# Kernel tuning notes

Hardware: AMD Instinct MI355X
Metric: run time of the kernel (lower is better)

The kernel has to match this reference:

```python
import jax, jax.numpy as jnp
import numpy as np

B, H, W, C = 32, 64, 64, 384
WS = 8            # window size (square)
NH = 12           # num heads
HD = C // NH      # head dim
SCALE = HD ** -0.5


def setup_inputs() -> dict:
    key = jax.random.key(0)
    ks = jax.random.split(key, 5)
    std = 0.02
    return {
        "x": jax.random.normal(ks[0], (B, H, W, C), dtype=jnp.float32),
        "w_qkv": jax.random.normal(ks[1], (C, 3 * C), dtype=jnp.float32) * std,
        "b_qkv": jnp.zeros((3 * C,), dtype=jnp.float32),
        "w_proj": jax.random.normal(ks[2], (C, C), dtype=jnp.float32) * std,
        "b_proj": jnp.zeros((C,), dtype=jnp.float32),
    }


def reference(x, w_qkv, b_qkv, w_proj, b_proj):
    b, h, w, c = x.shape
    nh_win, nw_win = h // WS, w // WS
    # window partition: (B, nh, WS, nw, WS, C) -> (B*nw_total, WS*WS, C)
    xw = x.reshape(b, nh_win, WS, nw_win, WS, c)
    xw = xw.transpose(0, 1, 3, 2, 4, 5).reshape(b * nh_win * nw_win, WS * WS, c)
    nW, T = xw.shape[0], WS * WS
    # qkv projection
    qkv = xw @ w_qkv + b_qkv                      # (nW, T, 3C)
    qkv = qkv.reshape(nW, T, 3, NH, HD).transpose(2, 0, 3, 1, 4)
    q, k, v = qkv[0], qkv[1], qkv[2]              # (nW, NH, T, HD)
    attn = jnp.einsum('wntd,wnsd->wnts', q, k) * SCALE
    attn = jax.nn.softmax(attn, axis=-1)
    out = jnp.einsum('wnts,wnsd->wntd', attn, v)  # (nW, NH, T, HD)
    out = out.transpose(0, 2, 1, 3).reshape(nW, T, c)
    out = out @ w_proj + b_proj
    # window reverse
    out = out.reshape(b, nh_win, nw_win, WS, WS, c)
    out = out.transpose(0, 1, 3, 2, 4, 5).reshape(b, h, w, c)
    return out
```

## Files before the change

kernel.cpp:

```cpp
#include <hip/hip_runtime.h>
#include <hip/hip_bf16.h>

typedef __bf16 bfv8 __attribute__((ext_vector_type(8)));
typedef float f32x4 __attribute__((ext_vector_type(4)));
typedef unsigned int u32;

#define MFMA(a,b,c) __builtin_amdgcn_mfma_f32_16x16x32_bf16((a),(b),(c),0,0,0)

constexpr int XW_LD = 392;

__global__ __launch_bounds__(256)
void prep_weights(const float* __restrict__ w_qkv, const float* __restrict__ w_proj,
                  unsigned short* __restrict__ qT, unsigned short* __restrict__ pT)
{
    int i = blockIdx.x * 256 + threadIdx.x;
    const int NQ = 1152 * 384;
    if (i < NQ) {
        int c = i / 384, k = i - c * 384;
        __bf16 h = (__bf16)w_qkv[k * 1152 + c];
        qT[i] = *(unsigned short*)&h;
    } else {
        int j = i - NQ;
        if (j < 384 * 384) {
            int c = j / 384, k = j - c * 384;
            __bf16 h = (__bf16)w_proj[k * 384 + c];
            pT[j] = *(unsigned short*)&h;
        }
    }
}

__device__ __forceinline__ u32 pkbf(float a, float b) {
    __bf16 x = (__bf16)a, y = (__bf16)b;
    unsigned short lo = *(unsigned short*)&x, hi = *(unsigned short*)&y;
    return ((u32)hi << 16) | lo;
}

__device__ __forceinline__ bfv8 conv_frag(u32 p00, u32 p01, u32 p10, u32 p11,
                                          int abase, bool selhi)
{
    union { u32 u[4]; bfv8 v; } cv;
    #pragma unroll
    for (int w = 0; w < 4; ++w) {
        const int addr = abase + (w >> 1) * 64;
        const int lo_ = __builtin_amdgcn_ds_bpermute(addr, (int)((w & 1) ? p01 : p00));
        const int hi_ = __builtin_amdgcn_ds_bpermute(addr, (int)((w & 1) ? p11 : p10));
        cv.u[w] = (u32)(selhi ? hi_ : lo_);
    }
    return cv.v;
}

__global__ __launch_bounds__(256, 3)
void win_attn(const float* __restrict__ x,
              const float* __restrict__ b_qkv,
              const float* __restrict__ b_proj,
              const unsigned short* __restrict__ qT_,
              const unsigned short* __restrict__ pT_,
              float* __restrict__ out)
{
    __shared__ __bf16 sX[64 * XW_LD];

    const __bf16* wqkvT  = (const __bf16*)qT_;
    const __bf16* wprojT = (const __bf16*)pT_;

    const int wid  = blockIdx.x;
    const int bb   = wid >> 6;
    const int wy   = (wid >> 3) & 7;
    const int wx   = wid & 7;
    const int tid  = threadIdx.x;
    const int lane = tid & 63;
    const int wv   = tid >> 6;
    const int lr   = lane & 15;
    const int lg   = lane >> 4;
    const int k8   = lg * 8;

    const size_t gbase = ((size_t)(bb * 64 + wy * 8) * 64 + wx * 8) * 384;

    {
        const float* xb = x + gbase;
        for (int i = tid; i < 64 * 96; i += 256) {
            int t  = i / 96;
            int c4 = (i - t * 96) * 4;
            const float4 v = *(const float4*)(xb + (size_t)((t >> 3) * 64 + (t & 7)) * 384 + c4);
            *(uint2*)&sX[t * XW_LD + c4] = make_uint2(pkbf(v.x, v.y), pkbf(v.z, v.w));
        }
    }
    __syncthreads();

    const int   abase = ((lg & 1) * 32 + lr) * 4;
    const bool  selhi = (lg & 2) != 0;
    const float SC    = 0.17677669529663687f;

    u32 opk0[4][2][2], opk1[4][2][2], opk2[4][2][2];

    auto head_body = [&](const int h, u32 (&opk_)[4][2][2]) {
        const int cQ = h * 32, cK = cQ + 384, cV = cQ + 768;

        f32x4 aq[2][4], ak[2][4], av[4][2];
        #pragma unroll
        for (int a = 0; a < 2; ++a)
            #pragma unroll
            for (int b = 0; b < 4; ++b) { aq[a][b] = f32x4{0,0,0,0}; ak[a][b] = f32x4{0,0,0,0}; av[b][a] = f32x4{0,0,0,0}; }

        const __bf16* wqp = wqkvT + (size_t)(cQ + lr) * 384 + k8;
        const __bf16* wkp = wqkvT + (size_t)(cK + lr) * 384 + k8;
        const __bf16* wvp = wqkvT + (size_t)(cV + lr) * 384 + k8;
        const __bf16* xp  = &sX[lr * XW_LD + k8];

        #pragma unroll 3
        for (int kk = 0; kk < 12; ++kk) {
            bfv8 xf[4], wqf[2], wkf[2], wvf[2];
            #pragma unroll
            for (int t4 = 0; t4 < 4; ++t4) xf[t4] = *(const bfv8*)(xp + t4 * 16 * XW_LD + kk * 32);
            #pragma unroll
            for (int hdt = 0; hdt < 2; ++hdt) {
                wqf[hdt] = *(const bfv8*)(wqp + (size_t)hdt * 16 * 384 + kk * 32);
                wkf[hdt] = *(const bfv8*)(wkp + (size_t)hdt * 16 * 384 + kk * 32);
                wvf[hdt] = *(const bfv8*)(wvp + (size_t)hdt * 16 * 384 + kk * 32);
            }
            __builtin_amdgcn_s_setprio(1);
            #pragma unroll
            for (int hdt = 0; hdt < 2; ++hdt)
                #pragma unroll
                for (int t4 = 0; t4 < 4; ++t4) {
                    aq[hdt][t4] = MFMA(wqf[hdt], xf[t4], aq[hdt][t4]);
                    ak[hdt][t4] = MFMA(wkf[hdt], xf[t4], ak[hdt][t4]);
                    av[t4][hdt] = MFMA(xf[t4], wvf[hdt], av[t4][hdt]);
                }
            __builtin_amdgcn_s_setprio(0);
        }

        float bqv[2][4], bkv[2][4], bvv[2];
        #pragma unroll
        for (int hdt = 0; hdt < 2; ++hdt) {
            #pragma unroll
            for (int r = 0; r < 4; ++r) {
                bqv[hdt][r] = b_qkv[cQ + hdt * 16 + lg * 4 + r];
                bkv[hdt][r] = b_qkv[cK + hdt * 16 + lg * 4 + r];
            }
            bvv[hdt] = b_qkv[cV + hdt * 16 + lr];
        }

        u32 pkQ[2][4][2], pkK[2][4][2], pkV[4][2][2];
        #pragma unroll
        for (int hdt = 0; hdt < 2; ++hdt)
            #pragma unroll
            for (int t4 = 0; t4 < 4; ++t4)
                #pragma unroll
                for (int p = 0; p < 2; ++p) {
                    pkQ[hdt][t4][p] = pkbf((aq[hdt][t4][2 * p] + bqv[hdt][2 * p]) * SC,
                                           (aq[hdt][t4][2 * p + 1] + bqv[hdt][2 * p + 1]) * SC);
                    pkK[hdt][t4][p] = pkbf(ak[hdt][t4][2 * p] + bkv[hdt][2 * p],
                                           ak[hdt][t4][2 * p + 1] + bkv[hdt][2 * p + 1]);
                    pkV[t4][hdt][p] = pkbf(av[t4][hdt][2 * p] + bvv[hdt],
                                           av[t4][hdt][2 * p + 1] + bvv[hdt]);
                }

        bfv8 Qf[4];
        #pragma unroll
        for (int qt = 0; qt < 4; ++qt)
            Qf[qt] = conv_frag(pkQ[0][qt][0], pkQ[0][qt][1], pkQ[1][qt][0], pkQ[1][qt][1], abase, selhi);
        f32x4 st[4][4];
        __builtin_amdgcn_s_setprio(1);
        #pragma unroll
        for (int kt = 0; kt < 4; ++kt) {
            const bfv8 kf = conv_frag(pkK[0][kt][0], pkK[0][kt][1], pkK[1][kt][0], pkK[1][kt][1], abase, selhi);
            #pragma unroll
            for (int qt = 0; qt < 4; ++qt) {
                f32x4 z{};
                st[kt][qt] = MFMA(kf, Qf[qt], z);
            }
        }
        __builtin_amdgcn_s_setprio(0);

        float rinv[4];
        #pragma unroll
        for (int qt = 0; qt < 4; ++qt) {
            float mx = -1e30f;
            #pragma unroll
            for (int kt = 0; kt < 4; ++kt)
                #pragma unroll
                for (int r = 0; r < 4; ++r) mx = fmaxf(mx, st[kt][qt][r]);
            mx = fmaxf(mx, __shfl_xor(mx, 16, 64));
            mx = fmaxf(mx, __shfl_xor(mx, 32, 64));
            float sum = 0.f;
            #pragma unroll
            for (int kt = 0; kt < 4; ++kt)
                #pragma unroll
                for (int r = 0; r < 4; ++r) { st[kt][qt][r] = __expf(st[kt][qt][r] - mx); sum += st[kt][qt][r]; }
            sum += __shfl_xor(sum, 16, 64);
            sum += __shfl_xor(sum, 32, 64);
            rinv[qt] = 1.f / sum;
        }
        u32 pkP[4][4][2];
        #pragma unroll
        for (int qt = 0; qt < 4; ++qt)
            #pragma unroll
            for (int kt = 0; kt < 4; ++kt)
                #pragma unroll
                for (int p = 0; p < 2; ++p)
                    pkP[qt][kt][p] = pkbf(st[kt][qt][2 * p] * rinv[qt], st[kt][qt][2 * p + 1] * rinv[qt]);

        bfv8 Vf[2][2];
        #pragma unroll
        for (int ks = 0; ks < 2; ++ks)
            #pragma unroll
            for (int hdt = 0; hdt < 2; ++hdt)
                Vf[ks][hdt] = conv_frag(pkV[2 * ks][hdt][0], pkV[2 * ks][hdt][1],
                                        pkV[2 * ks + 1][hdt][0], pkV[2 * ks + 1][hdt][1], abase, selhi);
        f32x4 o[4][2];
        #pragma unroll
        for (int qt = 0; qt < 4; ++qt)
            #pragma unroll
            for (int hdt = 0; hdt < 2; ++hdt) o[qt][hdt] = f32x4{0,0,0,0};
        #pragma unroll
        for (int qt = 0; qt < 4; ++qt) {
            bfv8 pf0 = conv_frag(pkP[qt][0][0], pkP[qt][0][1], pkP[qt][1][0], pkP[qt][1][1], abase, selhi);
            bfv8 pf1 = conv_frag(pkP[qt][2][0], pkP[qt][2][1], pkP[qt][3][0], pkP[qt][3][1], abase, selhi);
            __builtin_amdgcn_s_setprio(1);
            #pragma unroll
            for (int hdt = 0; hdt < 2; ++hdt) {
                o[qt][hdt] = MFMA(pf0, Vf[0][hdt], o[qt][hdt]);
                o[qt][hdt] = MFMA(pf1, Vf[1][hdt], o[qt][hdt]);
            }
            __builtin_amdgcn_s_setprio(0);
        }
        #pragma unroll
        for (int qt = 0; qt < 4; ++qt)
            #pragma unroll
            for (int hdt = 0; hdt < 2; ++hdt)
                #pragma unroll
                for (int p = 0; p < 2; ++p)
                    opk_[qt][hdt][p] = pkbf(o[qt][hdt][2 * p], o[qt][hdt][2 * p + 1]);
    };

    head_body(wv * 3 + 0, opk0);
    head_body(wv * 3 + 1, opk1);
    head_body(wv * 3 + 2, opk2);

    __syncthreads();

#define OWRITE(OPK, HL)                                                          \
    _Pragma("unroll") for (int qt = 0; qt < 4; ++qt)                             \
    _Pragma("unroll") for (int hdt = 0; hdt < 2; ++hdt)                          \
    _Pragma("unroll") for (int p = 0; p < 2; ++p) {                              \
        const u32 u = OPK[qt][hdt][p];                                           \
        const int row0 = qt * 16 + lg * 4 + 2 * p;                               \
        const int col  = (wv * 3 + (HL)) * 32 + hdt * 16 + lr;                   \
        unsigned short lo = (unsigned short)(u & 0xffff);                        \
        unsigned short hi = (unsigned short)(u >> 16);                           \
        sX[row0 * XW_LD + col]       = *(__bf16*)&lo;                            \
        sX[(row0 + 1) * XW_LD + col] = *(__bf16*)&hi;                            \
    }
    OWRITE(opk0, 0)
    OWRITE(opk1, 1)
    OWRITE(opk2, 2)
    __syncthreads();

    const int nb = wv * 96;
    f32x4 acc[4][6];
    {
        const __bf16* bp = wprojT + (size_t)(nb + lr) * 384 + k8;
        #pragma unroll
        for (int m = 0; m < 4; ++m)
            #pragma unroll
            for (int nt = 0; nt < 6; ++nt) acc[m][nt] = f32x4{0,0,0,0};
        #pragma unroll 2
        for (int kk = 0; kk < 12; ++kk) {
            bfv8 bfr[6];
            #pragma unroll
            for (int nt = 0; nt < 6; ++nt)
                bfr[nt] = *(const bfv8*)(bp + (size_t)nt * 16 * 384 + kk * 32);
            __builtin_amdgcn_s_setprio(1);
            #pragma unroll
            for (int m = 0; m < 4; ++m) {
                const bfv8 af = *(const bfv8*)&sX[(m * 16 + lr) * XW_LD + kk * 32 + k8];
                #pragma unroll
                for (int nt = 0; nt < 6; ++nt)
                    acc[m][nt] = MFMA(af, bfr[nt], acc[m][nt]);
            }
            __builtin_amdgcn_s_setprio(0);
        }
    }
    float bpj[6];
    #pragma unroll
    for (int nt = 0; nt < 6; ++nt) bpj[nt] = b_proj[nb + nt * 16 + lr];

    __syncthreads();
    float* sF = (float*)sX;
    float* ob = out + gbase;
    #pragma unroll
    for (int half = 0; half < 2; ++half) {
        #pragma unroll
        for (int mm = 0; mm < 2; ++mm) {
            const int m = half * 2 + mm;
            #pragma unroll
            for (int r = 0; r < 4; ++r) {
                const int row = mm * 16 + lg * 4 + r;
                #pragma unroll
                for (int nt = 0; nt < 6; ++nt)
                    sF[row * 384 + nb + nt * 16 + lr] = acc[m][nt][r] + bpj[nt];
            }
        }
        __syncthreads();
        for (int i = tid; i < 32 * 96; i += 256) {
            const int row = i / 96;
            const int c4  = (i - row * 96) * 4;
            const int t   = half * 32 + row;
            const float4 v = *(const float4*)&sF[row * 384 + c4];
            *(float4*)(ob + (size_t)((t >> 3) * 64 + (t & 7)) * 384 + c4) = v;
        }
        if (half == 0) __syncthreads();
    }
}

extern "C" void kernel_launch(void* const* d_in, const int* in_sizes, int n_in,
                              void* d_out, int out_size, void* d_ws, size_t ws_size,
                              hipStream_t stream)
{
    const float* x      = (const float*)d_in[0];
    const float* w_qkv  = (const float*)d_in[1];
    const float* b_qkv  = (const float*)d_in[2];
    const float* w_proj = (const float*)d_in[3];
    const float* b_proj = (const float*)d_in[4];
    float* out = (float*)d_out;

    unsigned short* qT = (unsigned short*)d_ws;
    unsigned short* pT = qT + 1152 * 384;

    const int NPREP = 1152 * 384 + 384 * 384;
    prep_weights<<<(NPREP + 255) / 256, 256, 0, stream>>>(w_qkv, w_proj, qT, pT);
    win_attn<<<2048, 256, 0, stream>>>(x, b_qkv, b_proj, qT, pT, out);
}
```

Baseline: 386.9 us.

## Stage weight tiles through LDS with async global_load_lds and double-buffered register prefetch

Weight fragments for the QKV and output projections are now fetched with global_load_lds into a per-wave LDS staging buffer. They are then read into registers through a software-pipelined double buffer, with explicit waitcnt and sched_barrier ordering so the next k-slice's loads overlap the current MFMAs. The per-head lambda becomes a non-unrolled loop, and occupancy hint drops from 3 to 2 blocks per CU to accommodate the extra LDS and registers. The aim is to hide global-load latency behind MFMA work, at the cost of lower occupancy and heavy reliance on hand-placed wait counts.

```diff
diff --git a/kernel.cpp b/kernel.cpp
--- a/kernel.cpp
+++ b/kernel.cpp
@@ -6,6 +6,7 @@
 typedef unsigned int u32;
 
 #define MFMA(a,b,c) __builtin_amdgcn_mfma_f32_16x16x32_bf16((a),(b),(c),0,0,0)
+#define SB() __builtin_amdgcn_sched_barrier(0)
 
 constexpr int XW_LD = 392;
 
@@ -35,6 +36,12 @@
     return ((u32)hi << 16) | lo;
 }
 
+__device__ __forceinline__ void gll16(const __bf16* g, __bf16* l) {
+    __builtin_amdgcn_global_load_lds(
+        (const __attribute__((address_space(1))) void*)g,
+        (__attribute__((address_space(3))) void*)l, 16, 0, 0);
+}
+
 __device__ __forceinline__ bfv8 conv_frag(u32 p00, u32 p01, u32 p10, u32 p11,
                                           int abase, bool selhi)
 {
@@ -49,7 +56,7 @@
     return cv.v;
 }
 
-__global__ __launch_bounds__(256, 3)
+__global__ __launch_bounds__(256, 2)
 void win_attn(const float* __restrict__ x,
               const float* __restrict__ b_qkv,
               const float* __restrict__ b_proj,
@@ -58,6 +65,7 @@
               float* __restrict__ out)
 {
     __shared__ __bf16 sX[64 * XW_LD];
+    __shared__ __bf16 sW[4][6][512];
 
     const __bf16* wqkvT  = (const __bf16*)qT_;
     const __bf16* wprojT = (const __bf16*)pT_;
@@ -72,6 +80,7 @@
     const int lr   = lane & 15;
     const int lg   = lane >> 4;
     const int k8   = lg * 8;
+    const int lane8 = lane * 8;
 
     const size_t gbase = ((size_t)(bb * 64 + wy * 8) * 64 + wx * 8) * 384;
 
@@ -92,42 +101,19 @@
 
     u32 opk0[4][2][2], opk1[4][2][2], opk2[4][2][2];
 
-    auto head_body = [&](const int h, u32 (&opk_)[4][2][2]) {
+    const __bf16* xp = &sX[lr * XW_LD + k8];
+
+    #pragma unroll 1
+    for (int hl = 0; hl < 3; ++hl) {
+        const int h  = wv * 3 + hl;
         const int cQ = h * 32, cK = cQ + 384, cV = cQ + 768;
 
-        f32x4 aq[2][4], ak[2][4], av[4][2];
-        #pragma unroll
-        for (int a = 0; a < 2; ++a)
-            #pragma unroll
-            for (int b = 0; b < 4; ++b) { aq[a][b] = f32x4{0,0,0,0}; ak[a][b] = f32x4{0,0,0,0}; av[b][a] = f32x4{0,0,0,0}; }
-
-        const __bf16* wqp = wqkvT + (size_t)(cQ + lr) * 384 + k8;
-        const __bf16* wkp = wqkvT + (size_t)(cK + lr) * 384 + k8;
-        const __bf16* wvp = wqkvT + (size_t)(cV + lr) * 384 + k8;
-        const __bf16* xp  = &sX[lr * XW_LD + k8];
-
-        #pragma unroll 3
-        for (int kk = 0; kk < 12; ++kk) {
-            bfv8 xf[4], wqf[2], wkf[2], wvf[2];
-            #pragma unroll
-            for (int t4 = 0; t4 < 4; ++t4) xf[t4] = *(const bfv8*)(xp + t4 * 16 * XW_LD + kk * 32);
-            #pragma unroll
-            for (int hdt = 0; hdt < 2; ++hdt) {
-                wqf[hdt] = *(const bfv8*)(wqp + (size_t)hdt * 16 * 384 + kk * 32);
-                wkf[hdt] = *(const bfv8*)(wkp + (size_t)hdt * 16 * 384 + kk * 32);
-                wvf[hdt] = *(const bfv8*)(wvp + (size_t)hdt * 16 * 384 + kk * 32);
-            }
-            __builtin_amdgcn_s_setprio(1);
+        const __bf16* gsrc[6];
+        #pragma unroll
+        for (int mat = 0; mat < 3; ++mat)
             #pragma unroll
             for (int hdt = 0; hdt < 2; ++hdt)
-                #pragma unroll
-                for (int t4 = 0; t4 < 4; ++t4) {
-                    aq[hdt][t4] = MFMA(wqf[hdt], xf[t4], aq[hdt][t4]);
-                    ak[hdt][t4] = MFMA(wkf[hdt], xf[t4], ak[hdt][t4]);
-                    av[t4][hdt] = MFMA(xf[t4], wvf[hdt], av[t4][hdt]);
-                }
-            __builtin_amdgcn_s_setprio(0);
-        }
+                gsrc[mat * 2 + hdt] = wqkvT + (size_t)(cQ + mat * 384 + hdt * 16 + lr) * 384 + k8;
 
         float bqv[2][4], bkv[2][4], bvv[2];
         #pragma unroll
@@ -139,6 +125,57 @@
             }
             bvv[hdt] = b_qkv[cV + hdt * 16 + lr];
         }
+
+        f32x4 aq[2][4], ak[2][4], av[4][2];
+        #pragma unroll
+        for (int a = 0; a < 2; ++a)
+            #pragma unroll
+            for (int b = 0; b < 4; ++b) { aq[a][b] = f32x4{0,0,0,0}; ak[a][b] = f32x4{0,0,0,0}; av[b][a] = f32x4{0,0,0,0}; }
+
+        bfv8 wA[6], xA[4], wB[6], xB[4];
+
+        #pragma unroll
+        for (int f = 0; f < 6; ++f) gll16(gsrc[f], &sW[wv][f][0]);
+        asm volatile("s_waitcnt vmcnt(0)" ::: "memory"); SB();
+        #pragma unroll
+        for (int f = 0; f < 6; ++f) wA[f] = *(const bfv8*)&sW[wv][f][lane8];
+        #pragma unroll
+        for (int t4 = 0; t4 < 4; ++t4) xA[t4] = *(const bfv8*)(xp + t4 * 16 * XW_LD);
+        asm volatile("s_waitcnt lgkmcnt(4)" ::: "memory"); SB();
+        #pragma unroll
+        for (int f = 0; f < 6; ++f) gll16(gsrc[f] + 32, &sW[wv][f][0]);
+
+#define QSTEP(WA, XA, WB, XB, KK) do {                                            \
+        const int kread = ((KK) + 1 < 12) ? (KK) + 1 : 11;                        \
+        const int kpre  = ((KK) + 2 < 12) ? (KK) + 2 : 11;                        \
+        asm volatile("s_waitcnt vmcnt(0)" ::: "memory"); SB();                    \
+        _Pragma("unroll") for (int f = 0; f < 6; ++f)                             \
+            WB[f] = *(const bfv8*)&sW[wv][f][lane8];                              \
+        _Pragma("unroll") for (int t4 = 0; t4 < 4; ++t4)                          \
+            XB[t4] = *(const bfv8*)(xp + t4 * 16 * XW_LD + kread * 32);           \
+        __builtin_amdgcn_s_setprio(1);                                            \
+        _Pragma("unroll") for (int t4 = 0; t4 < 4; ++t4) {                        \
+            aq[0][t4] = MFMA(WA[0], XA[t4], aq[0][t4]);                           \
+            ak[0][t4] = MFMA(WA[2], XA[t4], ak[0][t4]);                           \
+            av[t4][0] = MFMA(XA[t4], WA[4], av[t4][0]); }                         \
+        __builtin_amdgcn_s_setprio(0);                                            \
+        asm volatile("s_waitcnt lgkmcnt(4)" ::: "memory"); SB();                  \
+        _Pragma("unroll") for (int f = 0; f < 6; ++f)                             \
+            gll16(gsrc[f] + kpre * 32, &sW[wv][f][0]);                            \
+        __builtin_amdgcn_s_setprio(1);                                            \
+        _Pragma("unroll") for (int t4 = 0; t4 < 4; ++t4) {                        \
+            aq[1][t4] = MFMA(WA[1], XA[t4], aq[1][t4]);                           \
+            ak[1][t4] = MFMA(WA[3], XA[t4], ak[1][t4]);                           \
+            av[t4][1] = MFMA(XA[t4], WA[5], av[t4][1]); }                         \
+        __builtin_amdgcn_s_setprio(0);                                            \
+    } while (0)
+
+        #pragma unroll 1
+        for (int kp = 0; kp < 6; ++kp) {
+            QSTEP(wA, xA, wB, xB, 2 * kp);
+            QSTEP(wB, xB, wA, xA, 2 * kp + 1);
+        }
+#undef QSTEP
 
         u32 pkQ[2][4][2], pkK[2][4][2], pkV[4][2][2];
         #pragma unroll
@@ -224,18 +261,25 @@
             }
             __builtin_amdgcn_s_setprio(0);
         }
+        u32 tmp[4][2][2];
         #pragma unroll
         for (int qt = 0; qt < 4; ++qt)
             #pragma unroll
             for (int hdt = 0; hdt < 2; ++hdt)
                 #pragma unroll
                 for (int p = 0; p < 2; ++p)
-                    opk_[qt][hdt][p] = pkbf(o[qt][hdt][2 * p], o[qt][hdt][2 * p + 1]);
-    };
-
-    head_body(wv * 3 + 0, opk0);
-    head_body(wv * 3 + 1, opk1);
-    head_body(wv * 3 + 2, opk2);
+                    tmp[qt][hdt][p] = pkbf(o[qt][hdt][2 * p], o[qt][hdt][2 * p + 1]);
+        if (hl == 0) {
+            #pragma unroll
+            for (int qt = 0; qt < 4; ++qt) { opk0[qt][0][0]=tmp[qt][0][0]; opk0[qt][0][1]=tmp[qt][0][1]; opk0[qt][1][0]=tmp[qt][1][0]; opk0[qt][1][1]=tmp[qt][1][1]; }
+        } else if (hl == 1) {
+            #pragma unroll
+            for (int qt = 0; qt < 4; ++qt) { opk1[qt][0][0]=tmp[qt][0][0]; opk1[qt][0][1]=tmp[qt][0][1]; opk1[qt][1][0]=tmp[qt][1][0]; opk1[qt][1][1]=tmp[qt][1][1]; }
+        } else {
+            #pragma unroll
+            for (int qt = 0; qt < 4; ++qt) { opk2[qt][0][0]=tmp[qt][0][0]; opk2[qt][0][1]=tmp[qt][0][1]; opk2[qt][1][0]=tmp[qt][1][0]; opk2[qt][1][1]=tmp[qt][1][1]; }
+        }
+    }
 
     __syncthreads();
 
@@ -259,27 +303,57 @@
     const int nb = wv * 96;
     f32x4 acc[4][6];
     {
-        const __bf16* bp = wprojT + (size_t)(nb + lr) * 384 + k8;
+        const __bf16* psrc[6];
+        #pragma unroll
+        for (int nt = 0; nt < 6; ++nt)
+            psrc[nt] = wprojT + (size_t)(nb + nt * 16 + lr) * 384 + k8;
         #pragma unroll
         for (int m = 0; m < 4; ++m)
             #pragma unroll
             for (int nt = 0; nt < 6; ++nt) acc[m][nt] = f32x4{0,0,0,0};
-        #pragma unroll 2
-        for (int kk = 0; kk < 12; ++kk) {
-            bfv8 bfr[6];
-            #pragma unroll
-            for (int nt = 0; nt < 6; ++nt)
-                bfr[nt] = *(const bfv8*)(bp + (size_t)nt * 16 * 384 + kk * 32);
-            __builtin_amdgcn_s_setprio(1);
-            #pragma unroll
-            for (int m = 0; m < 4; ++m) {
-                const bfv8 af = *(const bfv8*)&sX[(m * 16 + lr) * XW_LD + kk * 32 + k8];
-                #pragma unroll
-                for (int nt = 0; nt < 6; ++nt)
-                    acc[m][nt] = MFMA(af, bfr[nt], acc[m][nt]);
-            }
-            __builtin_amdgcn_s_setprio(0);
-        }
+
+        bfv8 bA[6], aA[4], bB[6], aB[4];
+
+        #pragma unroll
+        for (int f = 0; f < 6; ++f) gll16(psrc[f], &sW[wv][f][0]);
+        asm volatile("s_waitcnt vmcnt(0)" ::: "memory"); SB();
+        #pragma unroll
+        for (int f = 0; f < 6; ++f) bA[f] = *(const bfv8*)&sW[wv][f][lane8];
+        #pragma unroll
+        for (int m = 0; m < 4; ++m) aA[m] = *(const bfv8*)(xp + m * 16 * XW_LD);
+        asm volatile("s_waitcnt lgkmcnt(4)" ::: "memory"); SB();
+        #pragma unroll
+        for (int f = 0; f < 6; ++f) gll16(psrc[f] + 32, &sW[wv][f][0]);
+
+#define PSTEP(BA, AA, BB, AB, KK) do {                                            \
+        const int kread = ((KK) + 1 < 12) ? (KK) + 1 : 11;                        \
+        const int kpre  = ((KK) + 2 < 12) ? (KK) + 2 : 11;                        \
+        asm volatile("s_waitcnt vmcnt(0)" ::: "memory"); SB();                    \
+        _Pragma("unroll") for (int f = 0; f < 6; ++f)                             \
+            BB[f] = *(const bfv8*)&sW[wv][f][lane8];                              \
+        _Pragma("unroll") for (int m = 0; m < 4; ++m)                             \
+            AB[m] = *(const bfv8*)(xp + m * 16 * XW_LD + kread * 32);             \
+        __builtin_amdgcn_s_setprio(1);                                            \
+        _Pragma("unroll") for (int m = 0; m < 2; ++m)                             \
+        _Pragma("unroll") for (int nt = 0; nt < 6; ++nt)                          \
+            acc[m][nt] = MFMA(AA[m], BA[nt], acc[m][nt]);                         \
+        __builtin_amdgcn_s_setprio(0);                                            \
+        asm volatile("s_waitcnt lgkmcnt(4)" ::: "memory"); SB();                  \
+        _Pragma("unroll") for (int f = 0; f < 6; ++f)                             \
+            gll16(psrc[f] + kpre * 32, &sW[wv][f][0]);                            \
+        __builtin_amdgcn_s_setprio(1);                                            \
+        _Pragma("unroll") for (int m = 2; m < 4; ++m)                             \
+        _Pragma("unroll") for (int nt = 0; nt < 6; ++nt)                          \
+            acc[m][nt] = MFMA(AA[m], BA[nt], acc[m][nt]);                         \
+        __builtin_amdgcn_s_setprio(0);                                            \
+    } while (0)
+
+        #pragma unroll 1
+        for (int kp = 0; kp < 6; ++kp) {
+            PSTEP(bA, aA, bB, aB, 2 * kp);
+            PSTEP(bB, aB, bA, aA, 2 * kp + 1);
+        }
+#undef PSTEP
     }
     float bpj[6];
     #pragma unroll
```

Result: slower. 419.1 us (+8.3%).
